# Optimization experiments

Measured on AMD Instinct MI355X. Metric: run time of the kernel, lower is better.

The kernel has to match this reference:

```python
import jax, jax.numpy as jnp
import numpy as np

T, B, N, F = 128, 8, 32, 128
H = 256  # hidden channels
DEG = 8


def setup_inputs() -> dict:
    key = jax.random.key(0)
    ks = jax.random.split(key, 8)
    data = jax.random.normal(ks[0], (T, B, N, F), jnp.float32)
    all_ohs = jax.random.normal(ks[1], (T, B, N, 8), jnp.float32)
    n0 = B * N * T
    n1 = B * N * (T // 2)
    edge_index0 = jax.random.randint(ks[2], (2, n0 * DEG), 0, n0)
    edge_index1 = jax.random.randint(ks[3], (2, n1 * DEG), 0, n1)
    def init(k, shape, fan):
        return jax.random.normal(k, shape, jnp.float32) / np.float32(np.sqrt(fan))
    W0 = init(ks[4], (2 * F, H), 2 * F); b0 = jnp.zeros((H,), jnp.float32)
    Wc0 = init(ks[5], (H, H, 5), H * 5); bc0 = jnp.zeros((H,), jnp.float32)
    W1 = init(ks[6], (2 * H, H), 2 * H); b1 = jnp.zeros((H,), jnp.float32)
    Wc1 = init(ks[7], (H, H, 5), H * 5); bc1 = jnp.zeros((H,), jnp.float32)
    return dict(data=data, all_ohs=all_ohs,
                edge_index0=edge_index0, edge_index1=edge_index1,
                W0=W0, b0=b0, Wc0=Wc0, bc0=bc0,
                W1=W1, b1=b1, Wc1=Wc1, bc1=bc1)


def edge_conv(x, edge_index, W, b):
    # PyG EdgeConv: out_i = max_{(j->i)} relu(Linear(cat[x_i, x_j - x_i]))
    src, dst = edge_index[0], edge_index[1]
    x_i = x[dst]           # [E, C] target features
    x_j = x[src]           # [E, C] source features
    msg = jax.nn.relu(jnp.concatenate([x_i, x_j - x_i], axis=-1) @ W + b)
    out = jax.ops.segment_max(msg, dst, num_segments=x.shape[0])
    return jnp.where(jnp.isneginf(out), 0.0, out)  # empty segments -> 0 (PyG fill)


def temp_conv(x, Wc, bc):
    # x: [BN, C, L]; Conv1d(k=5, pad=2) + relu + MaxPool1d(2)
    y = jax.lax.conv_general_dilated(x, Wc, (1,), [(2, 2)],
                                     dimension_numbers=('NCH', 'OIH', 'NCH'))
    y = jax.nn.relu(y + bc[None, :, None])
    L2 = y.shape[-1] // 2
    y = y[..., : L2 * 2].reshape(y.shape[0], y.shape[1], L2, 2)
    return jnp.max(y, axis=-1)


def reference(data, all_ohs, edge_index0, edge_index1,
              W0, b0, Wc0, bc0, W1, b1, Wc1, bc1):
    # 'fast' path, context=False: all_ohs unused beyond reshape
    length = data.shape[0]
    x = data.reshape(T, B * N, F).transpose(1, 0, 2).reshape(-1, F)  # [BN*T, F]
    layers = ((edge_index0, W0, b0, Wc0, bc0),
              (edge_index1, W1, b1, Wc1, bc1))
    for ei, W, b, Wc, bc in layers:
        x = edge_conv(x, ei, W, b)                       # [BN*length, C]
        x = x.reshape(-1, length, x.shape[-1])           # [BN, length, C]
        x = x.transpose(0, 2, 1)                         # [BN, C, length]
        x = temp_conv(x, Wc, bc)                         # [BN, C, length//2]
        length = x.shape[2]
        C = x.shape[1]
        x = x.transpose(0, 2, 1).reshape(-1, C)          # [BN*length, C]
    return x
```

## Files before the change

### kernel.cpp

```cpp
#include <hip/hip_runtime.h>
#include <hip/hip_bf16.h>
#include <math.h>

#define T0 128
#define BN 256
#define Ff 128
#define Hh 256
#define NODE0 32768
#define E0 262144
#define T1 64
#define NODE1 16384
#define E1 131072
#define CAP 48

typedef __attribute__((ext_vector_type(8))) short bhalf8;
typedef __attribute__((ext_vector_type(4))) float floatx4;

__device__ __forceinline__ unsigned short f2bf(float x) {
  union { float f; unsigned u; } v; v.f = x;
  unsigned r = v.u + 0x7fff + ((v.u >> 16) & 1);
  return (unsigned short)(r >> 16);
}
__device__ __forceinline__ float bf2f(unsigned short b) {
  union { unsigned u; float f; } v; v.u = ((unsigned)b) << 16;
  return v.f;
}

__global__ void k_prep(const float* __restrict__ data, unsigned short* __restrict__ X0b,
                       const float* __restrict__ W0, unsigned short* __restrict__ Wbot0,
                       unsigned short* __restrict__ Wd0,
                       const float* __restrict__ W1, unsigned short* __restrict__ Wbot1,
                       unsigned short* __restrict__ Wd1,
                       const float* __restrict__ Wc0, unsigned short* __restrict__ Wtb0,
                       const float* __restrict__ Wc1, unsigned short* __restrict__ Wtb1) {
  int b = blockIdx.x;
  int tid = threadIdx.x;
  if (b < 2048) {
    int idx = b * 256 + tid;
    int c8 = idx & 15;
    int r  = idx >> 4;
    int t  = r & (T0 - 1);
    int bn = r >> 7;
    const float* s = data + ((size_t)t * BN + bn) * Ff + c8 * 8;
    float4 a = *(const float4*)s;
    float4 bb = *(const float4*)(s + 4);
    unsigned short o[8];
    o[0] = f2bf(a.x); o[1] = f2bf(a.y); o[2] = f2bf(a.z); o[3] = f2bf(a.w);
    o[4] = f2bf(bb.x); o[5] = f2bf(bb.y); o[6] = f2bf(bb.z); o[7] = f2bf(bb.w);
    *(int4*)(X0b + ((size_t)(bn * T0 + t) * Ff + c8 * 8)) = *(int4*)o;
  } else if (b < 2176) {
    int idx = (b - 2048) * 256 + tid;
    int n = idx >> 7, k = idx & 127;
    float top = W0[(size_t)k * 256 + n];
    float bot = W0[(size_t)(128 + k) * 256 + n];
    Wbot0[idx] = f2bf(bot);
    Wd0[idx]   = f2bf(top - bot);
  } else if (b < 2432) {
    int idx = (b - 2176) * 256 + tid;
    int n = idx >> 8, k = idx & 255;
    float top = W1[(size_t)k * 256 + n];
    float bot = W1[(size_t)(256 + k) * 256 + n];
    Wbot1[idx] = f2bf(bot);
    Wd1[idx]   = f2bf(top - bot);
  } else if (b < 3712) {
    int idx = (b - 2432) * 256 + tid;
    int tap = idx >> 16, o = (idx >> 8) & 255, i = idx & 255;
    Wtb0[idx] = f2bf(Wc0[((size_t)o * 256 + i) * 5 + tap]);
  } else {
    int idx = (b - 3712) * 256 + tid;
    int tap = idx >> 16, o = (idx >> 8) & 255, i = idx & 255;
    Wtb1[idx] = f2bf(Wc1[((size_t)o * 256 + i) * 5 + tap]);
  }
}

__global__ void k_fill(const int* __restrict__ ei0, const int* __restrict__ ei1,
                       int* __restrict__ cnt0, int* __restrict__ cnt1,
                       int* __restrict__ slot0, int* __restrict__ slot1) {
  int e = blockIdx.x * 256 + threadIdx.x;
  if (e < E0) {
    int d = ei0[E0 + e];
    int p = atomicAdd(&cnt0[d], 1);
    if (p < CAP) slot0[(size_t)d * CAP + p] = ei0[e];
  } else {
    int e2 = e - E0;
    int d = ei1[E1 + e2];
    int p = atomicAdd(&cnt1[d], 1);
    if (p < CAP) slot1[(size_t)d * CAP + p] = ei1[e2];
  }
}

__global__ __launch_bounds__(256) void k_maxg(const unsigned short* __restrict__ Bm,
                                              const int* __restrict__ cnt,
                                              const int* __restrict__ slot,
                                              unsigned short* __restrict__ Mm) {
  int node = blockIdx.x * 4 + (threadIdx.x >> 6);
  int lane = threadIdx.x & 63;
  int n = cnt[node];
  if (n > CAP) n = CAP;
  const int* sl = slot + (size_t)node * CAP;
  float4 m = make_float4(-INFINITY, -INFINITY, -INFINITY, -INFINITY);
  int i = 0;
  for (; i + 4 <= n; i += 4) {
    int s0 = sl[i], s1 = sl[i + 1], s2 = sl[i + 2], s3 = sl[i + 3];
    ushort4 v0 = *(const ushort4*)(Bm + (size_t)s0 * 256 + lane * 4);
    ushort4 v1 = *(const ushort4*)(Bm + (size_t)s1 * 256 + lane * 4);
    ushort4 v2 = *(const ushort4*)(Bm + (size_t)s2 * 256 + lane * 4);
    ushort4 v3 = *(const ushort4*)(Bm + (size_t)s3 * 256 + lane * 4);
    m.x = fmaxf(fmaxf(fmaxf(m.x, bf2f(v0.x)), fmaxf(bf2f(v1.x), bf2f(v2.x))), bf2f(v3.x));
    m.y = fmaxf(fmaxf(fmaxf(m.y, bf2f(v0.y)), fmaxf(bf2f(v1.y), bf2f(v2.y))), bf2f(v3.y));
    m.z = fmaxf(fmaxf(fmaxf(m.z, bf2f(v0.z)), fmaxf(bf2f(v1.z), bf2f(v2.z))), bf2f(v3.z));
    m.w = fmaxf(fmaxf(fmaxf(m.w, bf2f(v0.w)), fmaxf(bf2f(v1.w), bf2f(v2.w))), bf2f(v3.w));
  }
  for (; i < n; ++i) {
    int s = sl[i];
    ushort4 v = *(const ushort4*)(Bm + (size_t)s * 256 + lane * 4);
    m.x = fmaxf(m.x, bf2f(v.x));
    m.y = fmaxf(m.y, bf2f(v.y));
    m.z = fmaxf(m.z, bf2f(v.z));
    m.w = fmaxf(m.w, bf2f(v.w));
  }
  ushort4 o;
  o.x = f2bf(m.x); o.y = f2bf(m.y); o.z = f2bf(m.z); o.w = f2bf(m.w);
  *(ushort4*)(Mm + (size_t)node * 256 + lane * 4) = o;
}

template <int MODE>
__global__ __launch_bounds__(256) void k_gemm(const unsigned short* __restrict__ A,
                                              const unsigned short* __restrict__ Wb,
                                              unsigned short* __restrict__ C, int K,
                                              const float* __restrict__ bias,
                                              const unsigned short* __restrict__ Mm) {
  __shared__ __align__(16) short A_lds[64 * 72];
  __shared__ __align__(16) short B_lds[128 * 72];
  int tid = threadIdx.x;
  int row0 = blockIdx.x * 64;
  int col0 = blockIdx.y * 128;
  int lane = tid & 63, wv = tid >> 6;
  int m16 = lane & 15, quad = lane >> 4;
  int sr = tid >> 3, sseg = tid & 7;

  floatx4 acc[8];
#pragma unroll
  for (int nt = 0; nt < 8; ++nt) acc[nt] = (floatx4){0.f, 0.f, 0.f, 0.f};

  for (int kb = 0; kb < K; kb += 64) {
    __syncthreads();
#pragma unroll
    for (int i = 0; i < 2; ++i) {
      int r = sr + i * 32;
      *(int4*)&A_lds[r * 72 + sseg * 8] =
          *(const int4*)(A + (size_t)(row0 + r) * K + kb + sseg * 8);
    }
#pragma unroll
    for (int i = 0; i < 4; ++i) {
      int r = sr + i * 32;
      *(int4*)&B_lds[r * 72 + sseg * 8] =
          *(const int4*)(Wb + (size_t)(col0 + r) * K + kb + sseg * 8);
    }
    __syncthreads();
#pragma unroll
    for (int ks = 0; ks < 2; ++ks) {
      bhalf8 a = *(const bhalf8*)&A_lds[(wv * 16 + m16) * 72 + ks * 32 + quad * 8];
#pragma unroll
      for (int nt = 0; nt < 8; ++nt) {
        bhalf8 b = *(const bhalf8*)&B_lds[(nt * 16 + m16) * 72 + ks * 32 + quad * 8];
        acc[nt] = __builtin_amdgcn_mfma_f32_16x16x32_bf16(a, b, acc[nt], 0, 0, 0);
      }
    }
  }

  int g0 = row0 + wv * 16 + quad * 4;
#pragma unroll
  for (int nt = 0; nt < 8; ++nt) {
    int c = col0 + nt * 16 + m16;
    float bv = (MODE == 1) ? bias[c] : 0.f;
#pragma unroll
    for (int r = 0; r < 4; ++r) {
      float v = acc[nt][r];
      if (MODE == 1) v = fmaxf(v + bv + bf2f(Mm[(size_t)(g0 + r) * 256 + c]), 0.f);
      C[(size_t)(g0 + r) * 256 + c] = f2bf(v);
    }
  }
}

template <int TRows, bool OUT_F32>
__global__ __launch_bounds__(256) void k_conv(const unsigned short* __restrict__ X,
                                              const unsigned short* __restrict__ Wtb,
                                              const float* __restrict__ bc,
                                              void* __restrict__ Yout) {
  __shared__ __align__(16) short A_lds[2 * 68 * 40];
  __shared__ __align__(16) short B_lds[320 * 40];
  int tid = threadIdx.x;
  int row0 = blockIdx.x * 128;
  int col0 = blockIdx.y * 64;
  int lane = tid & 63, wv = tid >> 6;
  int m16 = lane & 15, quad = lane >> 4;

  floatx4 acc[2][4];
#pragma unroll
  for (int s = 0; s < 2; ++s)
#pragma unroll
    for (int nt = 0; nt < 4; ++nt) acc[s][nt] = (floatx4){0.f, 0.f, 0.f, 0.f};

  for (int kb = 0; kb < 256; kb += 32) {
    __syncthreads();
    for (int u = tid; u < 544; u += 256) {
      int s = (u >= 272) ? 1 : 0;
      int v = u - s * 272;
      int rr = v >> 2, seg = v & 3;
      int base = row0 + s * 64;
      int lo = base & ~(TRows - 1);
      int g = base + rr - 2;
      int4 val = {0, 0, 0, 0};
      if (g >= lo && g < lo + TRows)
        val = *(const int4*)(X + (size_t)g * 256 + kb + seg * 8);
      *(int4*)&A_lds[(s * 68 + rr) * 40 + seg * 8] = val;
    }
#pragma unroll
    for (int i = 0; i < 5; ++i) {
      int u = tid + i * 256;
      int r = u >> 2, seg = u & 3;
      int tap = r >> 6, col = r & 63;
      *(int4*)&B_lds[r * 40 + seg * 8] =
          *(const int4*)(Wtb + (size_t)tap * 65536 + (size_t)(col0 + col) * 256 + kb + seg * 8);
    }
    __syncthreads();
#pragma unroll
    for (int tap = 0; tap < 5; ++tap) {
      bhalf8 a0 = *(const bhalf8*)&A_lds[(wv * 16 + m16 + tap) * 40 + quad * 8];
      bhalf8 a1 = *(const bhalf8*)&A_lds[(68 + wv * 16 + m16 + tap) * 40 + quad * 8];
#pragma unroll
      for (int nt = 0; nt < 4; ++nt) {
        bhalf8 b = *(const bhalf8*)&B_lds[((tap << 6) + nt * 16 + m16) * 40 + quad * 8];
        acc[0][nt] = __builtin_amdgcn_mfma_f32_16x16x32_bf16(a0, b, acc[0][nt], 0, 0, 0);
        acc[1][nt] = __builtin_amdgcn_mfma_f32_16x16x32_bf16(a1, b, acc[1][nt], 0, 0, 0);
      }
    }
  }

#pragma unroll
  for (int s = 0; s < 2; ++s) {
    int gbase = row0 + s * 64 + wv * 16 + quad * 4;
#pragma unroll
    for (int nt = 0; nt < 4; ++nt) {
      int c = col0 + nt * 16 + m16;
      float bv = bc[c];
      float y0 = fmaxf(acc[s][nt][0] + bv, 0.f);
      float y1 = fmaxf(acc[s][nt][1] + bv, 0.f);
      float y2 = fmaxf(acc[s][nt][2] + bv, 0.f);
      float y3 = fmaxf(acc[s][nt][3] + bv, 0.f);
      float p0 = fmaxf(y0, y1);
      float p1 = fmaxf(y2, y3);
      int o0 = gbase >> 1;
      if (OUT_F32) {
        float* Y = (float*)Yout;
        Y[(size_t)o0 * 256 + c] = p0;
        Y[(size_t)(o0 + 1) * 256 + c] = p1;
      } else {
        unsigned short* Y = (unsigned short*)Yout;
        Y[(size_t)o0 * 256 + c] = f2bf(p0);
        Y[(size_t)(o0 + 1) * 256 + c] = f2bf(p1);
      }
    }
  }
}

extern "C" void kernel_launch(void* const* d_in, const int* in_sizes, int n_in,
                              void* d_out, int out_size, void* d_ws, size_t ws_size,
                              hipStream_t stream) {
  const float* data = (const float*)d_in[0];
  const int* ei0 = (const int*)d_in[2];
  const int* ei1 = (const int*)d_in[3];
  const float* W0  = (const float*)d_in[4];
  const float* b0  = (const float*)d_in[5];
  const float* Wc0 = (const float*)d_in[6];
  const float* bc0 = (const float*)d_in[7];
  const float* W1  = (const float*)d_in[8];
  const float* b1  = (const float*)d_in[9];
  const float* Wc1 = (const float*)d_in[10];
  const float* bc1 = (const float*)d_in[11];
  float* out = (float*)d_out;

  char* base = (char*)d_ws;
  size_t off = 0;
  auto alloc = [&](size_t bytes) { void* p = base + off; off += (bytes + 255) & ~(size_t)255; return p; };
  unsigned short* X0b   = (unsigned short*)alloc((size_t)NODE0 * Ff * 2);
  unsigned short* Bm    = (unsigned short*)alloc((size_t)NODE0 * Hh * 2);
  unsigned short* Mm    = (unsigned short*)alloc((size_t)NODE0 * Hh * 2);
  unsigned short* X1b   = (unsigned short*)alloc((size_t)NODE0 * Hh * 2);
  unsigned short* Y0b   = (unsigned short*)alloc((size_t)NODE1 * Hh * 2);
  unsigned short* Wbot0 = (unsigned short*)alloc(256 * 128 * 2);
  unsigned short* Wd0   = (unsigned short*)alloc(256 * 128 * 2);
  unsigned short* Wbot1 = (unsigned short*)alloc(256 * 256 * 2);
  unsigned short* Wd1   = (unsigned short*)alloc(256 * 256 * 2);
  unsigned short* Wtb0  = (unsigned short*)alloc(5 * 65536 * 2);
  unsigned short* Wtb1  = (unsigned short*)alloc(5 * 65536 * 2);
  int* cnt0  = (int*)alloc(NODE0 * 4);
  int* cnt1  = (int*)alloc(NODE1 * 4);
  int* slot0 = (int*)alloc((size_t)NODE0 * CAP * 4);
  int* slot1 = (int*)alloc((size_t)NODE1 * CAP * 4);

  hipMemsetAsync(cnt0, 0, (NODE0 + NODE1) * sizeof(int), stream);

  k_prep<<<4992, 256, 0, stream>>>(data, X0b, W0, Wbot0, Wd0, W1, Wbot1, Wd1,
                                   Wc0, Wtb0, Wc1, Wtb1);
  k_fill<<<(E0 + E1) / 256, 256, 0, stream>>>(ei0, ei1, cnt0, cnt1, slot0, slot1);

  k_gemm<0><<<dim3(NODE0 / 64, 2), 256, 0, stream>>>(X0b, Wbot0, Bm, 128, nullptr, nullptr);
  k_maxg<<<NODE0 / 4, 256, 0, stream>>>(Bm, cnt0, slot0, Mm);
  k_gemm<1><<<dim3(NODE0 / 64, 2), 256, 0, stream>>>(X0b, Wd0, X1b, 128, b0, Mm);
  k_conv<128, false><<<dim3(NODE0 / 128, 4), 256, 0, stream>>>(X1b, Wtb0, bc0, Y0b);

  k_gemm<0><<<dim3(NODE1 / 64, 2), 256, 0, stream>>>(Y0b, Wbot1, Bm, 256, nullptr, nullptr);
  k_maxg<<<NODE1 / 4, 256, 0, stream>>>(Bm, cnt1, slot1, Mm);
  k_gemm<1><<<dim3(NODE1 / 64, 2), 256, 0, stream>>>(Y0b, Wd1, X1b, 256, b1, Mm);
  k_conv<64, true><<<dim3(NODE1 / 128, 4), 256, 0, stream>>>(X1b, Wtb1, bc1, out);
}
```

Measured before the change: 249.0 us.

## Merge prep and fill, fuse dual edge GEMMs, use 32x32 MFMA in conv

The prep and edge-fill kernels become a single launch. The two edge-conv GEMMs (Wbot and Wd) now run as one grid: the Wd half writes a bias-added fp32 partial, and the max-gather kernel adds it and applies relu, so the second GEMM launch and its Mm re-read are gone. The temporal conv switches from 16x16x32 to 32x32x16 bf16 MFMA tiles with a configurable column width per block, aiming for better operand reuse and fewer LDS reads. The trade-offs are extra fp32 traffic for P, larger accumulator register pressure in the conv, and fewer conv blocks in layer 0.

After: 226.8 us. 1.1x faster.

```diff
diff --git a/kernel.cpp b/kernel.cpp
--- a/kernel.cpp
+++ b/kernel.cpp
@@ -15,6 +15,7 @@
 
 typedef __attribute__((ext_vector_type(8))) short bhalf8;
 typedef __attribute__((ext_vector_type(4))) float floatx4;
+typedef __attribute__((ext_vector_type(16))) float floatx16;
 
 __device__ __forceinline__ unsigned short f2bf(float x) {
   union { float f; unsigned u; } v; v.f = x;
@@ -26,13 +27,16 @@
   return v.f;
 }
 
-__global__ void k_prep(const float* __restrict__ data, unsigned short* __restrict__ X0b,
-                       const float* __restrict__ W0, unsigned short* __restrict__ Wbot0,
-                       unsigned short* __restrict__ Wd0,
-                       const float* __restrict__ W1, unsigned short* __restrict__ Wbot1,
-                       unsigned short* __restrict__ Wd1,
-                       const float* __restrict__ Wc0, unsigned short* __restrict__ Wtb0,
-                       const float* __restrict__ Wc1, unsigned short* __restrict__ Wtb1) {
+__global__ void k_prepfill(const float* __restrict__ data, unsigned short* __restrict__ X0b,
+                           const float* __restrict__ W0, unsigned short* __restrict__ Wbot0,
+                           unsigned short* __restrict__ Wd0,
+                           const float* __restrict__ W1, unsigned short* __restrict__ Wbot1,
+                           unsigned short* __restrict__ Wd1,
+                           const float* __restrict__ Wc0, unsigned short* __restrict__ Wtb0,
+                           const float* __restrict__ Wc1, unsigned short* __restrict__ Wtb1,
+                           const int* __restrict__ ei0, const int* __restrict__ ei1,
+                           int* __restrict__ cnt0, int* __restrict__ cnt1,
+                           int* __restrict__ slot0, int* __restrict__ slot1) {
   int b = blockIdx.x;
   int tid = threadIdx.x;
   if (b < 2048) {
@@ -66,33 +70,98 @@
     int idx = (b - 2432) * 256 + tid;
     int tap = idx >> 16, o = (idx >> 8) & 255, i = idx & 255;
     Wtb0[idx] = f2bf(Wc0[((size_t)o * 256 + i) * 5 + tap]);
-  } else {
+  } else if (b < 4992) {
     int idx = (b - 3712) * 256 + tid;
     int tap = idx >> 16, o = (idx >> 8) & 255, i = idx & 255;
     Wtb1[idx] = f2bf(Wc1[((size_t)o * 256 + i) * 5 + tap]);
-  }
-}
-
-__global__ void k_fill(const int* __restrict__ ei0, const int* __restrict__ ei1,
-                       int* __restrict__ cnt0, int* __restrict__ cnt1,
-                       int* __restrict__ slot0, int* __restrict__ slot1) {
-  int e = blockIdx.x * 256 + threadIdx.x;
-  if (e < E0) {
-    int d = ei0[E0 + e];
-    int p = atomicAdd(&cnt0[d], 1);
-    if (p < CAP) slot0[(size_t)d * CAP + p] = ei0[e];
   } else {
-    int e2 = e - E0;
-    int d = ei1[E1 + e2];
-    int p = atomicAdd(&cnt1[d], 1);
-    if (p < CAP) slot1[(size_t)d * CAP + p] = ei1[e2];
-  }
-}
-
-__global__ __launch_bounds__(256) void k_maxg(const unsigned short* __restrict__ Bm,
-                                              const int* __restrict__ cnt,
-                                              const int* __restrict__ slot,
-                                              unsigned short* __restrict__ Mm) {
+    int e = (b - 4992) * 256 + tid;
+    if (e < E0) {
+      int d = ei0[E0 + e];
+      int p = atomicAdd(&cnt0[d], 1);
+      if (p < CAP) slot0[(size_t)d * CAP + p] = ei0[e];
+    } else {
+      int e2 = e - E0;
+      int d = ei1[E1 + e2];
+      int p = atomicAdd(&cnt1[d], 1);
+      if (p < CAP) slot1[(size_t)d * CAP + p] = ei1[e2];
+    }
+  }
+}
+
+__global__ __launch_bounds__(256) void k_gemm2(const unsigned short* __restrict__ A,
+                                               const unsigned short* __restrict__ Wbot,
+                                               const unsigned short* __restrict__ Wd,
+                                               unsigned short* __restrict__ Bm,
+                                               float* __restrict__ P, int K,
+                                               const float* __restrict__ bias) {
+  __shared__ __align__(16) short A_lds[64 * 72];
+  __shared__ __align__(16) short B_lds[128 * 72];
+  int tid = threadIdx.x;
+  int row0 = blockIdx.x * 64;
+  int g = blockIdx.y;
+  int col0 = (g & 1) * 128;
+  const unsigned short* Wb = (g < 2) ? Wbot : Wd;
+  int lane = tid & 63, wv = tid >> 6;
+  int m16 = lane & 15, quad = lane >> 4;
+  int sr = tid >> 3, sseg = tid & 7;
+
+  floatx4 acc[8];
+#pragma unroll
+  for (int nt = 0; nt < 8; ++nt) acc[nt] = (floatx4){0.f, 0.f, 0.f, 0.f};
+
+  for (int kb = 0; kb < K; kb += 64) {
+    __syncthreads();
+#pragma unroll
+    for (int i = 0; i < 2; ++i) {
+      int r = sr + i * 32;
+      *(int4*)&A_lds[r * 72 + sseg * 8] =
+          *(const int4*)(A + (size_t)(row0 + r) * K + kb + sseg * 8);
+    }
+#pragma unroll
+    for (int i = 0; i < 4; ++i) {
+      int r = sr + i * 32;
+      *(int4*)&B_lds[r * 72 + sseg * 8] =
+          *(const int4*)(Wb + (size_t)(col0 + r) * K + kb + sseg * 8);
+    }
+    __syncthreads();
+#pragma unroll
+    for (int ks = 0; ks < 2; ++ks) {
+      bhalf8 a = *(const bhalf8*)&A_lds[(wv * 16 + m16) * 72 + ks * 32 + quad * 8];
+#pragma unroll
+      for (int nt = 0; nt < 8; ++nt) {
+        bhalf8 b = *(const bhalf8*)&B_lds[(nt * 16 + m16) * 72 + ks * 32 + quad * 8];
+        acc[nt] = __builtin_amdgcn_mfma_f32_16x16x32_bf16(a, b, acc[nt], 0, 0, 0);
+      }
+    }
+  }
+
+  int g0 = row0 + wv * 16 + quad * 4;
+  if (g < 2) {
+#pragma unroll
+    for (int nt = 0; nt < 8; ++nt) {
+      int c = col0 + nt * 16 + m16;
+#pragma unroll
+      for (int r = 0; r < 4; ++r)
+        Bm[(size_t)(g0 + r) * 256 + c] = f2bf(acc[nt][r]);
+    }
+  } else {
+#pragma unroll
+    for (int nt = 0; nt < 8; ++nt) {
+      int c = col0 + nt * 16 + m16;
+      float bv = bias[c];
+#pragma unroll
+      for (int r = 0; r < 4; ++r)
+        P[(size_t)(g0 + r) * 256 + c] = acc[nt][r] + bv;
+    }
+  }
+}
+
+__global__ __launch_bounds__(256) void k_maxg2(const unsigned short* __restrict__ Bm,
+                                               const int* __restrict__ cnt,
+                                               const int* __restrict__ slot,
+                                               const float* __restrict__ P,
+                                               unsigned short* __restrict__ X1) {
   int node = blockIdx.x * 4 + (threadIdx.x >> 6);
   int lane = threadIdx.x & 63;
   int n = cnt[node];
@@ -119,88 +188,37 @@
     m.z = fmaxf(m.z, bf2f(v.z));
     m.w = fmaxf(m.w, bf2f(v.w));
   }
+  float4 p = *(const float4*)(P + (size_t)node * 256 + lane * 4);
   ushort4 o;
-  o.x = f2bf(m.x); o.y = f2bf(m.y); o.z = f2bf(m.z); o.w = f2bf(m.w);
-  *(ushort4*)(Mm + (size_t)node * 256 + lane * 4) = o;
-}
-
-template <int MODE>
-__global__ __launch_bounds__(256) void k_gemm(const unsigned short* __restrict__ A,
-                                              const unsigned short* __restrict__ Wb,
-                                              unsigned short* __restrict__ C, int K,
-                                              const float* __restrict__ bias,
-                                              const unsigned short* __restrict__ Mm) {
-  __shared__ __align__(16) short A_lds[64 * 72];
-  __shared__ __align__(16) short B_lds[128 * 72];
-  int tid = threadIdx.x;
-  int row0 = blockIdx.x * 64;
-  int col0 = blockIdx.y * 128;
-  int lane = tid & 63, wv = tid >> 6;
-  int m16 = lane & 15, quad = lane >> 4;
-  int sr = tid >> 3, sseg = tid & 7;
-
-  floatx4 acc[8];
-#pragma unroll
-  for (int nt = 0; nt < 8; ++nt) acc[nt] = (floatx4){0.f, 0.f, 0.f, 0.f};
-
-  for (int kb = 0; kb < K; kb += 64) {
-    __syncthreads();
-#pragma unroll
-    for (int i = 0; i < 2; ++i) {
-      int r = sr + i * 32;
-      *(int4*)&A_lds[r * 72 + sseg * 8] =
-          *(const int4*)(A + (size_t)(row0 + r) * K + kb + sseg * 8);
-    }
-#pragma unroll
-    for (int i = 0; i < 4; ++i) {
-      int r = sr + i * 32;
-      *(int4*)&B_lds[r * 72 + sseg * 8] =
-          *(const int4*)(Wb + (size_t)(col0 + r) * K + kb + sseg * 8);
-    }
-    __syncthreads();
-#pragma unroll
-    for (int ks = 0; ks < 2; ++ks) {
-      bhalf8 a = *(const bhalf8*)&A_lds[(wv * 16 + m16) * 72 + ks * 32 + quad * 8];
-#pragma unroll
-      for (int nt = 0; nt < 8; ++nt) {
-        bhalf8 b = *(const bhalf8*)&B_lds[(nt * 16 + m16) * 72 + ks * 32 + quad * 8];
-        acc[nt] = __builtin_amdgcn_mfma_f32_16x16x32_bf16(a, b, acc[nt], 0, 0, 0);
-      }
-    }
-  }
-
-  int g0 = row0 + wv * 16 + quad * 4;
-#pragma unroll
-  for (int nt = 0; nt < 8; ++nt) {
-    int c = col0 + nt * 16 + m16;
-    float bv = (MODE == 1) ? bias[c] : 0.f;
-#pragma unroll
-    for (int r = 0; r < 4; ++r) {
-      float v = acc[nt][r];
-      if (MODE == 1) v = fmaxf(v + bv + bf2f(Mm[(size_t)(g0 + r) * 256 + c]), 0.f);
-      C[(size_t)(g0 + r) * 256 + c] = f2bf(v);
-    }
-  }
-}
-
-template <int TRows, bool OUT_F32>
-__global__ __launch_bounds__(256) void k_conv(const unsigned short* __restrict__ X,
-                                              const unsigned short* __restrict__ Wtb,
-                                              const float* __restrict__ bc,
-                                              void* __restrict__ Yout) {
+  o.x = f2bf(fmaxf(p.x + m.x, 0.f));
+  o.y = f2bf(fmaxf(p.y + m.y, 0.f));
+  o.z = f2bf(fmaxf(p.z + m.z, 0.f));
+  o.w = f2bf(fmaxf(p.w + m.w, 0.f));
+  *(ushort4*)(X1 + (size_t)node * 256 + lane * 4) = o;
+}
+
+template <int TRows, int NT, bool OUT_F32>
+__global__ __launch_bounds__(256) void k_conv32(const unsigned short* __restrict__ X,
+                                                const unsigned short* __restrict__ Wtb,
+                                                const float* __restrict__ bc,
+                                                void* __restrict__ Yout) {
+  const int CB = NT * 64;
   __shared__ __align__(16) short A_lds[2 * 68 * 40];
-  __shared__ __align__(16) short B_lds[320 * 40];
+  __shared__ __align__(16) short B_lds[5 * CB * 40];
   int tid = threadIdx.x;
   int row0 = blockIdx.x * 128;
-  int col0 = blockIdx.y * 64;
+  int col0 = blockIdx.y * CB;
   int lane = tid & 63, wv = tid >> 6;
-  int m16 = lane & 15, quad = lane >> 4;
-
-  floatx4 acc[2][4];
-#pragma unroll
-  for (int s = 0; s < 2; ++s)
-#pragma unroll
-    for (int nt = 0; nt < 4; ++nt) acc[s][nt] = (floatx4){0.f, 0.f, 0.f, 0.f};
+  int l31 = lane & 31, khalf = lane >> 5;
+  int h = wv & 1, cpart = wv >> 1;
+
+  floatx16 acc[2][NT];
+#pragma unroll
+  for (int rt = 0; rt < 2; ++rt)
+#pragma unroll
+    for (int ct = 0; ct < NT; ++ct)
+#pragma unroll
+      for (int r = 0; r < 16; ++r) acc[rt][ct][r] = 0.f;
 
   for (int kb = 0; kb < 256; kb += 32) {
     __syncthreads();
@@ -210,56 +228,56 @@
       int rr = v >> 2, seg = v & 3;
       int base = row0 + s * 64;
       int lo = base & ~(TRows - 1);
-      int g = base + rr - 2;
+      int gr = base + rr - 2;
       int4 val = {0, 0, 0, 0};
-      if (g >= lo && g < lo + TRows)
-        val = *(const int4*)(X + (size_t)g * 256 + kb + seg * 8);
+      if (gr >= lo && gr < lo + TRows)
+        val = *(const int4*)(X + (size_t)gr * 256 + kb + seg * 8);
       *(int4*)&A_lds[(s * 68 + rr) * 40 + seg * 8] = val;
     }
 #pragma unroll
-    for (int i = 0; i < 5; ++i) {
+    for (int i = 0; i < 5 * NT; ++i) {
       int u = tid + i * 256;
       int r = u >> 2, seg = u & 3;
-      int tap = r >> 6, col = r & 63;
+      int tap = r / CB, col = r % CB;
       *(int4*)&B_lds[r * 40 + seg * 8] =
           *(const int4*)(Wtb + (size_t)tap * 65536 + (size_t)(col0 + col) * 256 + kb + seg * 8);
     }
     __syncthreads();
 #pragma unroll
     for (int tap = 0; tap < 5; ++tap) {
-      bhalf8 a0 = *(const bhalf8*)&A_lds[(wv * 16 + m16 + tap) * 40 + quad * 8];
-      bhalf8 a1 = *(const bhalf8*)&A_lds[(68 + wv * 16 + m16 + tap) * 40 + quad * 8];
-#pragma unroll
-      for (int nt = 0; nt < 4; ++nt) {
-        bhalf8 b = *(const bhalf8*)&B_lds[((tap << 6) + nt * 16 + m16) * 40 + quad * 8];
-        acc[0][nt] = __builtin_amdgcn_mfma_f32_16x16x32_bf16(a0, b, acc[0][nt], 0, 0, 0);
-        acc[1][nt] = __builtin_amdgcn_mfma_f32_16x16x32_bf16(a1, b, acc[1][nt], 0, 0, 0);
+#pragma unroll
+      for (int ks = 0; ks < 2; ++ks) {
+        int ko = ks * 16 + khalf * 8;
+        bhalf8 a[2];
+#pragma unroll
+        for (int rt = 0; rt < 2; ++rt)
+          a[rt] = *(const bhalf8*)&A_lds[(h * 68 + rt * 32 + l31 + tap) * 40 + ko];
+#pragma unroll
+        for (int ct = 0; ct < NT; ++ct) {
+          bhalf8 b = *(const bhalf8*)&B_lds[(tap * CB + cpart * NT * 32 + ct * 32 + l31) * 40 + ko];
+#pragma unroll
+          for (int rt = 0; rt < 2; ++rt)
+            acc[rt][ct] = __builtin_amdgcn_mfma_f32_32x32x16_bf16(a[rt], b, acc[rt][ct], 0, 0, 0);
+        }
       }
     }
   }
 
 #pragma unroll
-  for (int s = 0; s < 2; ++s) {
-    int gbase = row0 + s * 64 + wv * 16 + quad * 4;
-#pragma unroll
-    for (int nt = 0; nt < 4; ++nt) {
-      int c = col0 + nt * 16 + m16;
+  for (int rt = 0; rt < 2; ++rt) {
+#pragma unroll
+    for (int ct = 0; ct < NT; ++ct) {
+      int c = col0 + cpart * NT * 32 + ct * 32 + l31;
       float bv = bc[c];
-      float y0 = fmaxf(acc[s][nt][0] + bv, 0.f);
-      float y1 = fmaxf(acc[s][nt][1] + bv, 0.f);
-      float y2 = fmaxf(acc[s][nt][2] + bv, 0.f);
-      float y3 = fmaxf(acc[s][nt][3] + bv, 0.f);
-      float p0 = fmaxf(y0, y1);
-      float p1 = fmaxf(y2, y3);
-      int o0 = gbase >> 1;
-      if (OUT_F32) {
-        float* Y = (float*)Yout;
-        Y[(size_t)o0 * 256 + c] = p0;
-        Y[(size_t)(o0 + 1) * 256 + c] = p1;
-      } else {
-        unsigned short* Y = (unsigned short*)Yout;
-        Y[(size_t)o0 * 256 + c] = f2bf(p0);
-        Y[(size_t)(o0 + 1) * 256 + c] = f2bf(p1);
+#pragma unroll
+      for (int r = 0; r < 16; r += 2) {
+        int rowg = row0 + h * 64 + rt * 32 + 4 * khalf + 8 * (r >> 2) + (r & 3);
+        float y0 = fmaxf(acc[rt][ct][r] + bv, 0.f);
+        float y1 = fmaxf(acc[rt][ct][r + 1] + bv, 0.f);
+        float p = fmaxf(y0, y1);
+        int o = rowg >> 1;
+        if (OUT_F32) ((float*)Yout)[(size_t)o * 256 + c] = p;
+        else ((unsigned short*)Yout)[(size_t)o * 256 + c] = f2bf(p);
       }
     }
   }
@@ -286,7 +304,7 @@
   auto alloc = [&](size_t bytes) { void* p = base + off; off += (bytes + 255) & ~(size_t)255; return p; };
   unsigned short* X0b   = (unsigned short*)alloc((size_t)NODE0 * Ff * 2);
   unsigned short* Bm    = (unsigned short*)alloc((size_t)NODE0 * Hh * 2);
-  unsigned short* Mm    = (unsigned short*)alloc((size_t)NODE0 * Hh * 2);
+  float*          P     = (float*)alloc((size_t)NODE0 * Hh * 4);
   unsigned short* X1b   = (unsigned short*)alloc((size_t)NODE0 * Hh * 2);
   unsigned short* Y0b   = (unsigned short*)alloc((size_t)NODE1 * Hh * 2);
   unsigned short* Wbot0 = (unsigned short*)alloc(256 * 128 * 2);
@@ -302,17 +320,15 @@
 
   hipMemsetAsync(cnt0, 0, (NODE0 + NODE1) * sizeof(int), stream);
 
-  k_prep<<<4992, 256, 0, stream>>>(data, X0b, W0, Wbot0, Wd0, W1, Wbot1, Wd1,
-                                   Wc0, Wtb0, Wc1, Wtb1);
-  k_fill<<<(E0 + E1) / 256, 256, 0, stream>>>(ei0, ei1, cnt0, cnt1, slot0, slot1);
-
-  k_gemm<0><<<dim3(NODE0 / 64, 2), 256, 0, stream>>>(X0b, Wbot0, Bm, 128, nullptr, nullptr);
-  k_maxg<<<NODE0 / 4, 256, 0, stream>>>(Bm, cnt0, slot0, Mm);
-  k_gemm<1><<<dim3(NODE0 / 64, 2), 256, 0, stream>>>(X0b, Wd0, X1b, 128, b0, Mm);
-  k_conv<128, false><<<dim3(NODE0 / 128, 4), 256, 0, stream>>>(X1b, Wtb0, bc0, Y0b);
-
-  k_gemm<0><<<dim3(NODE1 / 64, 2), 256, 0, stream>>>(Y0b, Wbot1, Bm, 256, nullptr, nullptr);
-  k_maxg<<<NODE1 / 4, 256, 0, stream>>>(Bm, cnt1, slot1, Mm);
-  k_gemm<1><<<dim3(NODE1 / 64, 2), 256, 0, stream>>>(Y0b, Wd1, X1b, 256, b1, Mm);
-  k_conv<64, true><<<dim3(NODE1 / 128, 4), 256, 0, stream>>>(X1b, Wtb1, bc1, out);
-}
+  k_prepfill<<<6528, 256, 0, stream>>>(data, X0b, W0, Wbot0, Wd0, W1, Wbot1, Wd1,
+                                       Wc0, Wtb0, Wc1, Wtb1,
+                                       ei0, ei1, cnt0, cnt1, slot0, slot1);
+
+  k_gemm2<<<dim3(NODE0 / 64, 4), 256, 0, stream>>>(X0b, Wbot0, Wd0, Bm, P, 128, b0);
+  k_maxg2<<<NODE0 / 4, 256, 0, stream>>>(Bm, cnt0, slot0, P, X1b);
+  k_conv32<128, 2, false><<<dim3(NODE0 / 128, 2), 256, 0, stream>>>(X1b, Wtb0, bc0, Y0b);
+
+  k_gemm2<<<dim3(NODE1 / 64, 4), 256, 0, stream>>>(Y0b, Wbot1, Wd1, Bm, P, 256, b1);
+  k_maxg2<<<NODE1 / 4, 256, 0, stream>>>(Bm, cnt1, slot1, P, X1b);
+  k_conv32<64, 1, true><<<dim3(NODE1 / 128, 4), 256, 0, stream>>>(X1b, Wtb1, bc1, out);
+}
```
